# Kernel tuning notes

Measured on AMD Instinct MI355X. Metric: run time of the kernel, lower is better.

Reference implementation:

```python
import jax, jax.numpy as jnp
import numpy as np
from jax import lax

N = 2048
D_ENC = 64      # conv channels
D = 512         # node embedding dim (resnet18 feature dim)
K = 5           # max_num_neighbors
L_LAYERS = 4    # num_layers
ARENA = 32.0    # positions scaled to [0, ARENA)^2
R2 = 2.0        # radius^2 = (sqrt(2))^2


def setup_inputs() -> dict:
    key = jax.random.key(0)
    ks = jax.random.split(key, 9)
    imgs = jax.random.normal(ks[0], (N, 3, 64, 64), dtype=jnp.float32)
    pos = jax.random.uniform(ks[1], (N, 2), dtype=jnp.float32)  # scaled by ARENA inside
    conv_w = jax.random.normal(ks[2], (D_ENC, 3, 7, 7), dtype=jnp.float32) * 0.05
    conv_b = jnp.zeros((D_ENC,), dtype=jnp.float32)
    proj_w = jax.random.normal(ks[3], (D_ENC, D), dtype=jnp.float32) * (1.0 / np.sqrt(D_ENC))
    proj_b = jnp.zeros((D,), dtype=jnp.float32)
    w_self = jax.random.normal(ks[4], (L_LAYERS, D, D), dtype=jnp.float32) * (1.0 / np.sqrt(D))
    w_nbr = jax.random.normal(ks[5], (L_LAYERS, D, D), dtype=jnp.float32) * (1.0 / np.sqrt(D))
    b_gnn = jnp.zeros((L_LAYERS, D), dtype=jnp.float32)
    return {"imgs": imgs, "pos": pos, "conv_w": conv_w, "conv_b": conv_b,
            "proj_w": proj_w, "proj_b": proj_b,
            "w_self": w_self, "w_nbr": w_nbr, "b_gnn": b_gnn}


def _encode(imgs, conv_w, conv_b, proj_w, proj_b):
    # conv 7x7 stride 2 + relu + global avg pool + linear -> [N, D]
    x = lax.conv_general_dilated(imgs, conv_w, window_strides=(2, 2), padding="SAME",
                                 dimension_numbers=("NCHW", "OIHW", "NCHW"))
    x = jax.nn.relu(x + conv_b[None, :, None, None])
    x = x.mean(axis=(2, 3))                      # [N, D_ENC]
    return jax.nn.relu(x @ proj_w + proj_b)      # [N, D]


def _radius_knn(pos):
    # radius graph with radius sqrt(2), no self loops, capped at K neighbors
    p = pos * ARENA                              # [N, 2]
    d2 = jnp.sum((p[:, None, :] - p[None, :, :]) ** 2, axis=-1)  # [N, N]
    invalid = (d2 > R2) | jnp.eye(N, dtype=bool)
    d2m = jnp.where(invalid, jnp.inf, d2)
    neg_vals, idx = lax.top_k(-d2m, K)           # K nearest within radius
    valid = jnp.isfinite(neg_vals)               # [N, K]
    return idx, valid


def reference(imgs, pos, conv_w, conv_b, proj_w, proj_b, w_self, w_nbr, b_gnn):
    h = _encode(imgs, conv_w, conv_b, proj_w, proj_b)   # [N, D]
    idx, valid = _radius_knn(pos)                        # [N, K], [N, K]
    vmask = valid.astype(h.dtype)                        # [N, K]
    denom = jnp.maximum(vmask.sum(axis=1, keepdims=True), 1.0)  # [N, 1]
    for l in range(L_LAYERS):
        nbr = h[idx] * vmask[:, :, None]                 # [N, K, D] gather
        agg = nbr.sum(axis=1) / denom                    # mean over valid neighbors
        h = jax.nn.relu(h @ w_self[l] + agg @ w_nbr[l] + b_gnn[l])
    return h
```

## Files before the change

kernel.cpp:

```cpp
#include <hip/hip_runtime.h>


#define NNODES 2048

typedef __attribute__((ext_vector_type(8))) _Float16 half8;
typedef __attribute__((ext_vector_type(16))) float f32x16;

__device__ inline uint pack2h(float x, float y) {
  ushort a = __builtin_bit_cast(ushort, (_Float16)x);
  ushort b = __builtin_bit_cast(ushort, (_Float16)y);
  return (uint)a | ((uint)b << 16);
}

__global__ __launch_bounds__(256) void setup_kernel(
    const float* __restrict__ conv_w, const float* __restrict__ wsrc_s,
    const float* __restrict__ wsrc_n, const float* __restrict__ pos,
    ushort* __restrict__ wfrag, ushort* __restrict__ wT,
    int* __restrict__ nbr, float* __restrict__ den, float* __restrict__ enc) {
  __shared__ float4 smem4[1040];
  const int bid = blockIdx.x;
  const int tid = threadIdx.x;

  if (bid < 48) {
    int i = bid * 256 + tid;
    int j = i & 7;
    int l = (i >> 3) & 63;
    int q = i >> 9;
    int kb = q % 12, ct = q / 12;
    int g = 2 * kb + (l >> 5);
    int c = 32 * ct + (l & 31);
    float val = 0.f;
    if (g < 21 && j < 7) val = conv_w[c * 147 + g * 7 + j];
    wfrag[i] = __builtin_bit_cast(ushort, (_Float16)val);
    return;
  }

  if (bid < 560) {
    float(*s)[65] = (float(*)[65])smem4;
    int bid2 = bid - 48;
    int m = bid2 >> 6, kt = (bid2 >> 3) & 7, nt = bid2 & 7;
    const float* in = (m < 4) ? (wsrc_s + m * 262144) : (wsrc_n + (m - 4) * 262144);
    ushort* out = wT + m * 262144;
    int k0 = kt << 6, n0 = nt << 6;
#pragma unroll
    for (int rep = 0; rep < 4; ++rep) {
      int row = (rep << 4) + (tid >> 4);
      int c4 = (tid & 15) << 2;
      float4 v = *(const float4*)&in[(k0 + row) * 512 + n0 + c4];
      s[row][c4] = v.x; s[row][c4 + 1] = v.y; s[row][c4 + 2] = v.z; s[row][c4 + 3] = v.w;
    }
    __syncthreads();
#pragma unroll
    for (int rep = 0; rep < 4; ++rep) {
      int n = (rep << 4) + (tid >> 4);
      int k4 = (tid & 15) << 2;
      ushort4 o;
      o.x = __builtin_bit_cast(ushort, (_Float16)s[k4 + 0][n]);
      o.y = __builtin_bit_cast(ushort, (_Float16)s[k4 + 1][n]);
      o.z = __builtin_bit_cast(ushort, (_Float16)s[k4 + 2][n]);
      o.w = __builtin_bit_cast(ushort, (_Float16)s[k4 + 3][n]);
      *(ushort4*)&out[(n0 + n) * 512 + k0 + k4] = o;
    }
    return;
  }

  {
    float* s_d2 = (float*)smem4;
    int* s_idx = (int*)(s_d2 + NNODES);
    int* s_cnt = (int*)(s_idx + NNODES);
    const int i = bid - 560;
    if (tid < 16) {
      float4 z4 = {0.f, 0.f, 0.f, 0.f};
      ((float4*)(enc + i * 64))[tid] = z4;
    }
    if (tid == 0) *s_cnt = 0;
    __syncthreads();
    const float px = pos[2 * i] * 32.f, py = pos[2 * i + 1] * 32.f;
#pragma unroll
    for (int r = 0; r < 8; ++r) {
      int j = tid + (r << 8);
      float2 q = ((const float2*)pos)[j];
      float dx = q.x * 32.f - px, dy = q.y * 32.f - py;
      float d2 = dx * dx + dy * dy;
      if (d2 <= 2.0f && j != i) {
        int slot = atomicAdd(s_cnt, 1);
        s_d2[slot] = d2;
        s_idx[slot] = j;
      }
    }
    __syncthreads();
    if (tid < 64) {
      const int lane = tid;
      const int cnt = *s_cnt;
      int nf = 0;
#pragma unroll
      for (int k = 0; k < 5; ++k) {
        float best = 1e30f;
        int bslot = 0x7fffffff;
        for (int e = lane; e < cnt; e += 64) {
          float d = s_d2[e];
          if (d < best) { best = d; bslot = e; }
        }
#pragma unroll
        for (int off = 1; off < 64; off <<= 1) {
          float od = __shfl_xor(best, off);
          int os = __shfl_xor(bslot, off);
          if (od < best || (od == best && os < bslot)) { best = od; bslot = os; }
        }
        bool got = (best < 1e30f);
        if (lane == 0) nbr[i * 5 + k] = got ? s_idx[bslot] : -1;
        if (got) { s_d2[bslot] = 1e30f; ++nf; }
      }
      if (lane == 0) den[i] = 1.f / (float)(nf > 0 ? nf : 1);
    }
  }
}

__global__ __launch_bounds__(256, 3) void conv_pool_kernel(
    const float* __restrict__ imgs, const ushort* __restrict__ wfrag,
    const float* __restrict__ cb, float* __restrict__ enc) {
  __shared__ int4 s_all[2599];
  ushort* s_img = (ushort*)s_all;
  const half8* swf8 = (const half8*)((char*)s_all + 15984);
  float* s_pool = (float*)((char*)s_all + 40560);

  const int n = blockIdx.x >> 1;
  const int r0half = blockIdx.x & 1;
  const int wy = 32 * r0half - 2;
  const int tid = threadIdx.x;
  const int lane = tid & 63;
  const int w = tid >> 6;
  const int hi = lane >> 5;
  const int lo = lane & 31;

  int4 z = {0, 0, 0, 0};
  for (int i = tid; i < 999; i += 256) s_all[i] = z;
  __syncthreads();

  const int4* wf4 = (const int4*)wfrag;
  int4* swf4 = (int4*)((char*)s_all + 15984);
#pragma unroll
  for (int r = 0; r < 6; ++r) swf4[tid + r * 256] = wf4[tid + r * 256];

  const float4* src = (const float4*)(imgs + (size_t)n * 12288);
  for (int i = tid; i < 1776; i += 256) {
    int ic = i / 592;
    int rem = i - ic * 592;
    int li = rem >> 4, xq = rem & 15;
    int iy = wy + li;
    if (iy >= 0 && iy < 64) {
      float4 v = src[(ic * 64 + iy) * 16 + xq];
      int d = (ic * 37 + li) * 72 + (xq << 2) + 2;
      ((uint*)s_img)[d >> 1] = pack2h(v.x, v.y);
      ((uint*)s_img)[(d >> 1) + 1] = pack2h(v.z, v.w);
    }
  }

  int aoff[12];
#pragma unroll
  for (int kb = 0; kb < 12; ++kb) {
    int g = 2 * kb + hi;
    if (g > 20) g = 20;
    int ic = g / 7, ky = g - ic * 7;
    aoff[kb] = (ic * 37 + ky) * 144 + 4 * lo + w * 1152;
  }
  const float bias0 = cb[lo];
  const float bias1 = cb[32 + lo];
  float pool0 = 0.f, pool1 = 0.f;
  __syncthreads();

  const char* sb = (const char*)s_img;
  union F { half8 v; uint u[4]; };

#define LOADF(F0, F1, B0, B1, KB, TPADD) do {                       \
    const char* p_ = sb + aoff[KB] + (TPADD);                       \
    F0.u[0] = *(const uint*)(p_);       F0.u[1] = *(const uint*)(p_ + 4);   \
    F0.u[2] = *(const uint*)(p_ + 8);   F0.u[3] = *(const uint*)(p_ + 12);  \
    F1.u[0] = *(const uint*)(p_ + 288); F1.u[1] = *(const uint*)(p_ + 292); \
    F1.u[2] = *(const uint*)(p_ + 296); F1.u[3] = *(const uint*)(p_ + 300); \
    B0 = swf8[(KB) * 64 + lane];        B1 = swf8[(12 + (KB)) * 64 + lane]; \
  } while (0)

#pragma unroll
  for (int tp = 0; tp < 2; ++tp) {
    const int tpadd = tp * 576;
    f32x16 a0 = {}, a1 = {}, a2 = {}, a3 = {};
    F f0a, f1a, f0b, f1b;
    half8 b0a, b1a, b0b, b1b;
    LOADF(f0a, f1a, b0a, b1a, 0, tpadd);
#pragma unroll
    for (int kb = 0; kb < 12; kb += 2) {
      LOADF(f0b, f1b, b0b, b1b, kb + 1, tpadd);
      a0 = __builtin_amdgcn_mfma_f32_32x32x16_f16(f0a.v, b0a, a0, 0, 0, 0);
      a1 = __builtin_amdgcn_mfma_f32_32x32x16_f16(f0a.v, b1a, a1, 0, 0, 0);
      a2 = __builtin_amdgcn_mfma_f32_32x32x16_f16(f1a.v, b0a, a2, 0, 0, 0);
      a3 = __builtin_amdgcn_mfma_f32_32x32x16_f16(f1a.v, b1a, a3, 0, 0, 0);
      if (kb + 2 < 12) LOADF(f0a, f1a, b0a, b1a, kb + 2, tpadd);
      a0 = __builtin_amdgcn_mfma_f32_32x32x16_f16(f0b.v, b0b, a0, 0, 0, 0);
      a1 = __builtin_amdgcn_mfma_f32_32x32x16_f16(f0b.v, b1b, a1, 0, 0, 0);
      a2 = __builtin_amdgcn_mfma_f32_32x32x16_f16(f1b.v, b0b, a2, 0, 0, 0);
      a3 = __builtin_amdgcn_mfma_f32_32x32x16_f16(f1b.v, b1b, a3, 0, 0, 0);
    }
    float s0 = 0.f, s1 = 0.f;
#pragma unroll
    for (int r = 0; r < 16; ++r) {
      s0 += fmaxf(a0[r] + bias0, 0.f) + fmaxf(a2[r] + bias0, 0.f);
      s1 += fmaxf(a1[r] + bias1, 0.f) + fmaxf(a3[r] + bias1, 0.f);
    }
    pool0 += s0;
    pool1 += s1;
  }
#undef LOADF

  pool0 += __shfl_xor(pool0, 32);
  pool1 += __shfl_xor(pool1, 32);
  if (lane < 32) {
    s_pool[w * 64 + lo] = pool0;
    s_pool[w * 64 + 32 + lo] = pool1;
  }
  __syncthreads();
  if (tid < 64) {
    float s = s_pool[tid] + s_pool[64 + tid] + s_pool[128 + tid] + s_pool[192 + tid];
    atomicAdd(&enc[n * 64 + tid], s * (1.f / 1024.f));
  }
}

__global__ __launch_bounds__(256) void proj_kernel(
    const float* __restrict__ enc, const float* __restrict__ pw,
    const float* __restrict__ pb, ushort* __restrict__ h16) {
  int c = ((blockIdx.x & 1) << 8) | threadIdx.x;
  int r0 = (blockIdx.x >> 1) << 3;
  float bias = pb[c];
  float acc[8];
#pragma unroll
  for (int r = 0; r < 8; ++r) acc[r] = bias;
#pragma unroll 4
  for (int k = 0; k < 64; ++k) {
    float w = pw[k * 512 + c];
#pragma unroll
    for (int r = 0; r < 8; ++r) acc[r] = fmaf(enc[(r0 + r) * 64 + k], w, acc[r]);
  }
#pragma unroll
  for (int r = 0; r < 8; ++r)
    h16[(r0 + r) * 512 + c] = __builtin_bit_cast(ushort, (_Float16)fmaxf(acc[r], 0.f));
}

__global__ __launch_bounds__(256) void gnn_gemm_kernel(
    const ushort* __restrict__ h16, const int* __restrict__ nbr,
    const float* __restrict__ den,
    const ushort* __restrict__ Ws, const ushort* __restrict__ Wn,
    const float* __restrict__ bias, ushort* __restrict__ hout,
    float* __restrict__ fout, int final_layer) {
  __shared__ ushort s_lds[2][16384];
  __shared__ int s_nbr[320];
  __shared__ float s_den[64];
  const int tid = threadIdx.x;
  const int lane = tid & 63;
  const int hi = lane >> 5, lo = lane & 31;
  const int wu = __builtin_amdgcn_readfirstlane(tid >> 6);
  const int wr = wu >> 1, wc = wu & 1;
  const int bm = blockIdx.x >> 3, bn = blockIdx.x & 7;
  const int r0 = bm << 6, c0 = bn << 6;

  if (tid < 80) ((int4*)s_nbr)[tid] = ((const int4*)(nbr + r0 * 5))[tid];
  else if (tid < 96) ((float4*)s_den)[tid - 80] = ((const float4*)(den + r0))[tid - 80];
  __syncthreads();

  const int grow = tid >> 2, gseg = tid & 3;
  int gj[5];
  uint gm[5];
#pragma unroll
  for (int k = 0; k < 5; ++k) {
    int j = s_nbr[grow * 5 + k];
    gm[k] = (j >= 0) ? 0xFFFFFFFFu : 0u;
    gj[k] = (j >= 0) ? j : 0;
  }
  half8 den8;
  {
    _Float16 dh = (_Float16)s_den[grow];
#pragma unroll
    for (int e = 0; e < 8; ++e) den8[e] = dh;
  }

  union GU { half8 v; uint u[4]; };
  GU ga[5][2];

  auto GATHER = [&](int it) {
    const ushort* hb = h16 + (it << 6) + gseg * 16;
#pragma unroll
    for (int k = 0; k < 5; ++k) {
      const half8* p = (const half8*)(hb + gj[k] * 512);
      ga[k][0].v = p[0];
      ga[k][1].v = p[1];
    }
  };
  auto COMBINE = [&](int buf) {
#pragma unroll
    for (int part = 0; part < 2; ++part) {
      GU t0, t1, t2, t3, t4;
#pragma unroll
      for (int j2 = 0; j2 < 4; ++j2) {
        t0.u[j2] = ga[0][part].u[j2] & gm[0];
        t1.u[j2] = ga[1][part].u[j2] & gm[1];
        t2.u[j2] = ga[2][part].u[j2] & gm[2];
        t3.u[j2] = ga[3][part].u[j2] & gm[3];
        t4.u[j2] = ga[4][part].u[j2] & gm[4];
      }
      half8 s = ((t0.v + t1.v) + (t2.v + t3.v)) + t4.v;
      s = s * den8;
      *(half8*)&s_lds[buf][4096 + (2 * gseg + part) * 512 + grow * 8] = s;
    }
  };
  auto STAGE = [&](int buf, int it) {
    int k0 = it << 6;
    const ushort* ph = h16 + (r0 + lane) * 512 + k0 + 8 * wu;
    const ushort* ps = Ws + (c0 + lane) * 512 + k0 + 8 * wu;
    const ushort* pn = Wn + (c0 + lane) * 512 + k0 + 8 * wu;
    ushort* lb = &s_lds[buf][wu << 9];
#define GLDS(SRC, DST) __builtin_amdgcn_global_load_lds( \
      (const __attribute__((address_space(1))) void*)(SRC), \
      (__attribute__((address_space(3))) void*)(DST), 16, 0, 0)
    GLDS(ph, lb);            GLDS(ph + 32, lb + 2048);
    GLDS(ps, lb + 8192);     GLDS(ps + 32, lb + 10240);
    GLDS(pn, lb + 12288);    GLDS(pn + 32, lb + 14336);
#undef GLDS
  };

  f32x16 accS = {}, accN = {};
  GATHER(0);
  STAGE(0, 0);
  COMBINE(0);
  __syncthreads();
  int cur = 0;
  for (int it = 0; it < 8; ++it) {
    if (it < 7) {
      GATHER(it + 1);
      STAGE(cur ^ 1, it + 1);
    }
    const half8* pAh = (const half8*)&s_lds[cur][0];
    const half8* pAg = (const half8*)&s_lds[cur][4096];
    const half8* pBs = (const half8*)&s_lds[cur][8192];
    const half8* pBn = (const half8*)&s_lds[cur][12288];
#pragma unroll
    for (int ks = 0; ks < 4; ++ks) {
      int gi = (2 * ks + hi) * 64;
      half8 ah = pAh[gi + 32 * wr + lo];
      half8 bs = pBs[gi + 32 * wc + lo];
      accS = __builtin_amdgcn_mfma_f32_32x32x16_f16(ah, bs, accS, 0, 0, 0);
      half8 ag = pAg[gi + 32 * wr + lo];
      half8 bn2 = pBn[gi + 32 * wc + lo];
      accN = __builtin_amdgcn_mfma_f32_32x32x16_f16(ag, bn2, accN, 0, 0, 0);
    }
    if (it < 7) COMBINE(cur ^ 1);
    __syncthreads();
    cur ^= 1;
  }

  const int col = c0 + 32 * wc + lo;
  const float b = bias[col];
#pragma unroll
  for (int r = 0; r < 16; ++r) {
    int row = r0 + 32 * wr + (r & 3) + ((r >> 2) << 3) + (hi << 2);
    float v = fmaxf(accS[r] + accN[r] + b, 0.f);
    if (final_layer) fout[row * 512 + col] = v;
    else hout[row * 512 + col] = __builtin_bit_cast(ushort, (_Float16)v);
  }
}

extern "C" void kernel_launch(void* const* d_in, const int* in_sizes, int n_in,
                              void* d_out, int out_size, void* d_ws, size_t ws_size,
                              hipStream_t stream) {
  const float* imgs   = (const float*)d_in[0];
  const float* pos    = (const float*)d_in[1];
  const float* conv_w = (const float*)d_in[2];
  const float* conv_b = (const float*)d_in[3];
  const float* proj_w = (const float*)d_in[4];
  const float* proj_b = (const float*)d_in[5];
  const float* w_self = (const float*)d_in[6];
  const float* w_nbr  = (const float*)d_in[7];
  const float* b_gnn  = (const float*)d_in[8];

  char* ws = (char*)d_ws;
  ushort* wfrag = (ushort*)(ws);
  float*  enc   = (float*) (ws + 32768);
  ushort* h16a  = (ushort*)(ws + 557056);
  ushort* h16b  = (ushort*)(ws + 2654208);
  ushort* wT16  = (ushort*)(ws + 6848512);
  int*    nbr   = (int*)   (ws + 11042816);
  float*  den   = (float*) (ws + 11083776);

  setup_kernel<<<2608, 256, 0, stream>>>(conv_w, w_self, w_nbr, pos,
                                         wfrag, wT16, nbr, den, enc);
  conv_pool_kernel<<<2 * NNODES, 256, 0, stream>>>(imgs, wfrag, conv_b, enc);
  proj_kernel<<<512, 256, 0, stream>>>(enc, proj_w, proj_b, h16a);

  for (int l = 0; l < 4; ++l) {
    ushort* hin  = (l & 1) ? h16b : h16a;
    ushort* hnew = (l & 1) ? h16a : h16b;
    gnn_gemm_kernel<<<256, 256, 0, stream>>>(
        hin, nbr, den, wT16 + l * 262144, wT16 + (4 + l) * 262144,
        b_gnn + l * 512, hnew, (float*)d_out, (l == 3) ? 1 : 0);
  }
}
```

Before: 141.7 us.

## Load GNN GEMM operands directly into registers instead of staging through LDS

In the GNN GEMM kernel, the h, W_self and W_nbr tiles are now read from global memory straight into double-buffered registers, replacing the global_load_lds staging into shared memory. Only the aggregated neighbour tile still goes through LDS. This shrinks the LDS footprint and removes the LDS reads for those operands, but each wave now loads its own copy of tiles that are shared across waves, which raises register pressure and global/L2 traffic. The conv LDS fragment loads are also rewritten as 8-byte memcpys to encourage wider ds_read instructions.

```diff
diff --git a/kernel.cpp b/kernel.cpp
--- a/kernel.cpp
+++ b/kernel.cpp
@@ -172,13 +172,14 @@
   const char* sb = (const char*)s_img;
   union F { half8 v; uint u[4]; };
 
-#define LOADF(F0, F1, B0, B1, KB, TPADD) do {                       \
-    const char* p_ = sb + aoff[KB] + (TPADD);                       \
-    F0.u[0] = *(const uint*)(p_);       F0.u[1] = *(const uint*)(p_ + 4);   \
-    F0.u[2] = *(const uint*)(p_ + 8);   F0.u[3] = *(const uint*)(p_ + 12);  \
-    F1.u[0] = *(const uint*)(p_ + 288); F1.u[1] = *(const uint*)(p_ + 292); \
-    F1.u[2] = *(const uint*)(p_ + 296); F1.u[3] = *(const uint*)(p_ + 300); \
-    B0 = swf8[(KB) * 64 + lane];        B1 = swf8[(12 + (KB)) * 64 + lane]; \
+#define LOADF(F0, F1, B0, B1, KB, TPADD) do {                                 \
+    const char* p_ = (const char*)__builtin_assume_aligned(                   \
+        sb + aoff[KB] + (TPADD), 4);                                          \
+    __builtin_memcpy(&F0.u[0], p_, 8);                                        \
+    __builtin_memcpy(&F0.u[2], p_ + 8, 8);                                    \
+    __builtin_memcpy(&F1.u[0], p_ + 288, 8);                                  \
+    __builtin_memcpy(&F1.u[2], p_ + 296, 8);                                  \
+    B0 = swf8[(KB) * 64 + lane];        B1 = swf8[(12 + (KB)) * 64 + lane];   \
   } while (0)
 
 #pragma unroll
@@ -251,7 +252,7 @@
     const ushort* __restrict__ Ws, const ushort* __restrict__ Wn,
     const float* __restrict__ bias, ushort* __restrict__ hout,
     float* __restrict__ fout, int final_layer) {
-  __shared__ ushort s_lds[2][16384];
+  __shared__ ushort s_ag[2][4096];
   __shared__ int s_nbr[320];
   __shared__ float s_den[64];
   const int tid = threadIdx.x;
@@ -308,53 +309,50 @@
       }
       half8 s = ((t0.v + t1.v) + (t2.v + t3.v)) + t4.v;
       s = s * den8;
-      *(half8*)&s_lds[buf][4096 + (2 * gseg + part) * 512 + grow * 8] = s;
+      *(half8*)&s_ag[buf][(2 * gseg + part) * 512 + grow * 8] = s;
     }
   };
-  auto STAGE = [&](int buf, int it) {
-    int k0 = it << 6;
-    const ushort* ph = h16 + (r0 + lane) * 512 + k0 + 8 * wu;
-    const ushort* ps = Ws + (c0 + lane) * 512 + k0 + 8 * wu;
-    const ushort* pn = Wn + (c0 + lane) * 512 + k0 + 8 * wu;
-    ushort* lb = &s_lds[buf][wu << 9];
-#define GLDS(SRC, DST) __builtin_amdgcn_global_load_lds( \
-      (const __attribute__((address_space(1))) void*)(SRC), \
-      (__attribute__((address_space(3))) void*)(DST), 16, 0, 0)
-    GLDS(ph, lb);            GLDS(ph + 32, lb + 2048);
-    GLDS(ps, lb + 8192);     GLDS(ps + 32, lb + 10240);
-    GLDS(pn, lb + 12288);    GLDS(pn + 32, lb + 14336);
-#undef GLDS
-  };
+
+  const ushort* pA  = h16 + (r0 + 32 * wr + lo) * 512 + 8 * hi;
+  const ushort* pBs = Ws  + (c0 + 32 * wc + lo) * 512 + 8 * hi;
+  const ushort* pBn = Wn  + (c0 + 32 * wc + lo) * 512 + 8 * hi;
+
+  half8 rA[2][4], rS[2][4], rN[2][4];
+#define LOADABR(P, IT) do {                                                   \
+    int kk_ = (IT) << 6;                                                      \
+    _Pragma("unroll")                                                         \
+    for (int ks_ = 0; ks_ < 4; ++ks_) {                                       \
+      rA[P][ks_] = *(const half8*)(pA  + kk_ + 16 * ks_);                     \
+      rS[P][ks_] = *(const half8*)(pBs + kk_ + 16 * ks_);                     \
+      rN[P][ks_] = *(const half8*)(pBn + kk_ + 16 * ks_);                     \
+    }                                                                         \
+  } while (0)
 
   f32x16 accS = {}, accN = {};
   GATHER(0);
-  STAGE(0, 0);
+  LOADABR(0, 0);
   COMBINE(0);
   __syncthreads();
   int cur = 0;
+#pragma unroll
   for (int it = 0; it < 8; ++it) {
+    const int p = it & 1;
     if (it < 7) {
       GATHER(it + 1);
-      STAGE(cur ^ 1, it + 1);
-    }
-    const half8* pAh = (const half8*)&s_lds[cur][0];
-    const half8* pAg = (const half8*)&s_lds[cur][4096];
-    const half8* pBs = (const half8*)&s_lds[cur][8192];
-    const half8* pBn = (const half8*)&s_lds[cur][12288];
+      LOADABR(1 - p, it + 1);
+    }
+    const half8* agp = (const half8*)s_ag[cur];
 #pragma unroll
     for (int ks = 0; ks < 4; ++ks) {
-      int gi = (2 * ks + hi) * 64;
-      half8 ah = pAh[gi + 32 * wr + lo];
-      half8 bs = pBs[gi + 32 * wc + lo];
-      accS = __builtin_amdgcn_mfma_f32_32x32x16_f16(ah, bs, accS, 0, 0, 0);
-      half8 ag = pAg[gi + 32 * wr + lo];
-      half8 bn2 = pBn[gi + 32 * wc + lo];
-      accN = __builtin_amdgcn_mfma_f32_32x32x16_f16(ag, bn2, accN, 0, 0, 0);
+      accS = __builtin_amdgcn_mfma_f32_32x32x16_f16(rA[p][ks], rS[p][ks], accS, 0, 0, 0);
+      half8 ag = agp[(2 * ks + hi) * 64 + 32 * wr + lo];
+      accN = __builtin_amdgcn_mfma_f32_32x32x16_f16(ag, rN[p][ks], accN, 0, 0, 0);
     }
     if (it < 7) COMBINE(cur ^ 1);
     __syncthreads();
     cur ^= 1;
   }
+#undef LOADABR
 
   const int col = c0 + 32 * wc + lo;
   const float b = bias[col];
```

Measured after the change: 151.0 us. 1.07x slower.

## Split-K the GNN GEMM into two halves with a separate reduce kernel

Applied to the files above, without the earlier changes.

The GNN layer GEMM is split along K into two halves, doubling the grid from 256 to 512 blocks so more of the device's compute units are occupied. Each half writes fp32 partial sums to a workspace buffer, and a new reduce kernel adds the two partials plus bias, applies ReLU and writes fp16 or final fp32 output. This adds an extra launch per layer and extra global traffic for the partials. The conv LDS fragment loads are also rewritten as 8-byte memcpys so the compiler can emit wider LDS reads.

```diff
diff --git a/kernel.cpp b/kernel.cpp
--- a/kernel.cpp
+++ b/kernel.cpp
@@ -172,13 +172,14 @@
   const char* sb = (const char*)s_img;
   union F { half8 v; uint u[4]; };
 
-#define LOADF(F0, F1, B0, B1, KB, TPADD) do {                       \
-    const char* p_ = sb + aoff[KB] + (TPADD);                       \
-    F0.u[0] = *(const uint*)(p_);       F0.u[1] = *(const uint*)(p_ + 4);   \
-    F0.u[2] = *(const uint*)(p_ + 8);   F0.u[3] = *(const uint*)(p_ + 12);  \
-    F1.u[0] = *(const uint*)(p_ + 288); F1.u[1] = *(const uint*)(p_ + 292); \
-    F1.u[2] = *(const uint*)(p_ + 296); F1.u[3] = *(const uint*)(p_ + 300); \
-    B0 = swf8[(KB) * 64 + lane];        B1 = swf8[(12 + (KB)) * 64 + lane]; \
+#define LOADF(F0, F1, B0, B1, KB, TPADD) do {                                 \
+    const char* p_ = (const char*)__builtin_assume_aligned(                   \
+        sb + aoff[KB] + (TPADD), 4);                                          \
+    __builtin_memcpy(&F0.u[0], p_, 8);                                        \
+    __builtin_memcpy(&F0.u[2], p_ + 8, 8);                                    \
+    __builtin_memcpy(&F1.u[0], p_ + 288, 8);                                  \
+    __builtin_memcpy(&F1.u[2], p_ + 296, 8);                                  \
+    B0 = swf8[(KB) * 64 + lane];        B1 = swf8[(12 + (KB)) * 64 + lane];   \
   } while (0)
 
 #pragma unroll
@@ -249,8 +250,7 @@
     const ushort* __restrict__ h16, const int* __restrict__ nbr,
     const float* __restrict__ den,
     const ushort* __restrict__ Ws, const ushort* __restrict__ Wn,
-    const float* __restrict__ bias, ushort* __restrict__ hout,
-    float* __restrict__ fout, int final_layer) {
+    float* __restrict__ part) {
   __shared__ ushort s_lds[2][16384];
   __shared__ int s_nbr[320];
   __shared__ float s_den[64];
@@ -259,8 +259,10 @@
   const int hi = lane >> 5, lo = lane & 31;
   const int wu = __builtin_amdgcn_readfirstlane(tid >> 6);
   const int wr = wu >> 1, wc = wu & 1;
-  const int bm = blockIdx.x >> 3, bn = blockIdx.x & 7;
+  const int split = blockIdx.x >> 8;
+  const int bm = (blockIdx.x >> 3) & 31, bn = blockIdx.x & 7;
   const int r0 = bm << 6, c0 = bn << 6;
+  const int itb = split << 2;
 
   if (tid < 80) ((int4*)s_nbr)[tid] = ((const int4*)(nbr + r0 * 5))[tid];
   else if (tid < 96) ((float4*)s_den)[tid - 80] = ((const float4*)(den + r0))[tid - 80];
@@ -296,19 +298,19 @@
   };
   auto COMBINE = [&](int buf) {
 #pragma unroll
-    for (int part = 0; part < 2; ++part) {
+    for (int part2 = 0; part2 < 2; ++part2) {
       GU t0, t1, t2, t3, t4;
 #pragma unroll
       for (int j2 = 0; j2 < 4; ++j2) {
-        t0.u[j2] = ga[0][part].u[j2] & gm[0];
-        t1.u[j2] = ga[1][part].u[j2] & gm[1];
-        t2.u[j2] = ga[2][part].u[j2] & gm[2];
-        t3.u[j2] = ga[3][part].u[j2] & gm[3];
-        t4.u[j2] = ga[4][part].u[j2] & gm[4];
+        t0.u[j2] = ga[0][part2].u[j2] & gm[0];
+        t1.u[j2] = ga[1][part2].u[j2] & gm[1];
+        t2.u[j2] = ga[2][part2].u[j2] & gm[2];
+        t3.u[j2] = ga[3][part2].u[j2] & gm[3];
+        t4.u[j2] = ga[4][part2].u[j2] & gm[4];
       }
       half8 s = ((t0.v + t1.v) + (t2.v + t3.v)) + t4.v;
       s = s * den8;
-      *(half8*)&s_lds[buf][4096 + (2 * gseg + part) * 512 + grow * 8] = s;
+      *(half8*)&s_lds[buf][4096 + (2 * gseg + part2) * 512 + grow * 8] = s;
     }
   };
   auto STAGE = [&](int buf, int it) {
@@ -327,15 +329,15 @@
   };
 
   f32x16 accS = {}, accN = {};
-  GATHER(0);
-  STAGE(0, 0);
+  GATHER(itb);
+  STAGE(0, itb);
   COMBINE(0);
   __syncthreads();
   int cur = 0;
-  for (int it = 0; it < 8; ++it) {
-    if (it < 7) {
-      GATHER(it + 1);
-      STAGE(cur ^ 1, it + 1);
+  for (int it = 0; it < 4; ++it) {
+    if (it < 3) {
+      GATHER(itb + it + 1);
+      STAGE(cur ^ 1, itb + it + 1);
     }
     const half8* pAh = (const half8*)&s_lds[cur][0];
     const half8* pAg = (const half8*)&s_lds[cur][4096];
@@ -351,19 +353,41 @@
       half8 bn2 = pBn[gi + 32 * wc + lo];
       accN = __builtin_amdgcn_mfma_f32_32x32x16_f16(ag, bn2, accN, 0, 0, 0);
     }
-    if (it < 7) COMBINE(cur ^ 1);
+    if (it < 3) COMBINE(cur ^ 1);
     __syncthreads();
     cur ^= 1;
   }
 
   const int col = c0 + 32 * wc + lo;
-  const float b = bias[col];
+  float* dst = part + (size_t)split * (NNODES * 512);
 #pragma unroll
   for (int r = 0; r < 16; ++r) {
     int row = r0 + 32 * wr + (r & 3) + ((r >> 2) << 3) + (hi << 2);
-    float v = fmaxf(accS[r] + accN[r] + b, 0.f);
-    if (final_layer) fout[row * 512 + col] = v;
-    else hout[row * 512 + col] = __builtin_bit_cast(ushort, (_Float16)v);
+    dst[row * 512 + col] = accS[r] + accN[r];
+  }
+}
+
+__global__ __launch_bounds__(256) void gnn_reduce_kernel(
+    const float* __restrict__ part, const float* __restrict__ bg,
+    ushort* __restrict__ hout, float* __restrict__ fout, int final_layer) {
+  int i = blockIdx.x * 256 + threadIdx.x;
+  float4 a = ((const float4*)part)[i];
+  float4 b = ((const float4*)part)[i + 262144];
+  float4 bb = ((const float4*)bg)[i & 127];
+  float4 o;
+  o.x = fmaxf(a.x + b.x + bb.x, 0.f);
+  o.y = fmaxf(a.y + b.y + bb.y, 0.f);
+  o.z = fmaxf(a.z + b.z + bb.z, 0.f);
+  o.w = fmaxf(a.w + b.w + bb.w, 0.f);
+  if (final_layer) {
+    ((float4*)fout)[i] = o;
+  } else {
+    ushort4 h;
+    h.x = __builtin_bit_cast(ushort, (_Float16)o.x);
+    h.y = __builtin_bit_cast(ushort, (_Float16)o.y);
+    h.z = __builtin_bit_cast(ushort, (_Float16)o.z);
+    h.w = __builtin_bit_cast(ushort, (_Float16)o.w);
+    ((ushort4*)hout)[i] = h;
   }
 }
 
@@ -388,6 +412,7 @@
   ushort* wT16  = (ushort*)(ws + 6848512);
   int*    nbr   = (int*)   (ws + 11042816);
   float*  den   = (float*) (ws + 11083776);
+  float*  part  = (float*) (ws + 11534336);
 
   setup_kernel<<<2608, 256, 0, stream>>>(conv_w, w_self, w_nbr, pos,
                                          wfrag, wT16, nbr, den, enc);
@@ -397,8 +422,9 @@
   for (int l = 0; l < 4; ++l) {
     ushort* hin  = (l & 1) ? h16b : h16a;
     ushort* hnew = (l & 1) ? h16a : h16b;
-    gnn_gemm_kernel<<<256, 256, 0, stream>>>(
-        hin, nbr, den, wT16 + l * 262144, wT16 + (4 + l) * 262144,
-        b_gnn + l * 512, hnew, (float*)d_out, (l == 3) ? 1 : 0);
-  }
-}
+    gnn_gemm_kernel<<<512, 256, 0, stream>>>(
+        hin, nbr, den, wT16 + l * 262144, wT16 + (4 + l) * 262144, part);
+    gnn_reduce_kernel<<<1024, 256, 0, stream>>>(
+        part, b_gnn + l * 512, hnew, (float*)d_out, (l == 3) ? 1 : 0);
+  }
+}
```

After: 149.3 us. 5.3% more time.

## Fuse four GNN layer launches into one cooperative kernel with grid sync

Applied to the files above, without the earlier changes.

Replaces the four per-layer GEMM launches with a single cooperative kernel that loops over the layers and uses a grid-wide barrier plus threadfence between them. The goal is to remove the launch overhead and inter-kernel gaps of three extra launches. It also rewrites the conv fragment LDS loads as 8-byte memcpy with an alignment hint, so the compiler can emit wider loads. The cost is a grid sync per layer, and the grid of 256 blocks must fit co-resident for the cooperative launch.

```diff
diff --git a/kernel.cpp b/kernel.cpp
--- a/kernel.cpp
+++ b/kernel.cpp
@@ -1,4 +1,5 @@
 #include <hip/hip_runtime.h>
+#include <hip/hip_cooperative_groups.h>
 
 
 #define NNODES 2048
@@ -172,13 +173,14 @@
   const char* sb = (const char*)s_img;
   union F { half8 v; uint u[4]; };
 
-#define LOADF(F0, F1, B0, B1, KB, TPADD) do {                       \
-    const char* p_ = sb + aoff[KB] + (TPADD);                       \
-    F0.u[0] = *(const uint*)(p_);       F0.u[1] = *(const uint*)(p_ + 4);   \
-    F0.u[2] = *(const uint*)(p_ + 8);   F0.u[3] = *(const uint*)(p_ + 12);  \
-    F1.u[0] = *(const uint*)(p_ + 288); F1.u[1] = *(const uint*)(p_ + 292); \
-    F1.u[2] = *(const uint*)(p_ + 296); F1.u[3] = *(const uint*)(p_ + 300); \
-    B0 = swf8[(KB) * 64 + lane];        B1 = swf8[(12 + (KB)) * 64 + lane]; \
+#define LOADF(F0, F1, B0, B1, KB, TPADD) do {                                 \
+    const char* p_ = (const char*)__builtin_assume_aligned(                   \
+        sb + aoff[KB] + (TPADD), 4);                                          \
+    __builtin_memcpy(&F0.u[0], p_, 8);                                        \
+    __builtin_memcpy(&F0.u[2], p_ + 8, 8);                                    \
+    __builtin_memcpy(&F1.u[0], p_ + 288, 8);                                  \
+    __builtin_memcpy(&F1.u[2], p_ + 296, 8);                                  \
+    B0 = swf8[(KB) * 64 + lane];        B1 = swf8[(12 + (KB)) * 64 + lane];   \
   } while (0)
 
 #pragma unroll
@@ -245,12 +247,11 @@
     h16[(r0 + r) * 512 + c] = __builtin_bit_cast(ushort, (_Float16)fmaxf(acc[r], 0.f));
 }
 
-__global__ __launch_bounds__(256) void gnn_gemm_kernel(
-    const ushort* __restrict__ h16, const int* __restrict__ nbr,
-    const float* __restrict__ den,
-    const ushort* __restrict__ Ws, const ushort* __restrict__ Wn,
-    const float* __restrict__ bias, ushort* __restrict__ hout,
-    float* __restrict__ fout, int final_layer) {
+__global__ __launch_bounds__(256) void gnn_layers_kernel(
+    ushort* __restrict__ h16a, ushort* __restrict__ h16b,
+    const int* __restrict__ nbr, const float* __restrict__ den,
+    const ushort* __restrict__ wT16, const float* __restrict__ b_gnn,
+    float* __restrict__ fout) {
   __shared__ ushort s_lds[2][16384];
   __shared__ int s_nbr[320];
   __shared__ float s_den[64];
@@ -285,85 +286,100 @@
   union GU { half8 v; uint u[4]; };
   GU ga[5][2];
 
-  auto GATHER = [&](int it) {
-    const ushort* hb = h16 + (it << 6) + gseg * 16;
-#pragma unroll
-    for (int k = 0; k < 5; ++k) {
-      const half8* p = (const half8*)(hb + gj[k] * 512);
-      ga[k][0].v = p[0];
-      ga[k][1].v = p[1];
-    }
-  };
-  auto COMBINE = [&](int buf) {
-#pragma unroll
-    for (int part = 0; part < 2; ++part) {
-      GU t0, t1, t2, t3, t4;
-#pragma unroll
-      for (int j2 = 0; j2 < 4; ++j2) {
-        t0.u[j2] = ga[0][part].u[j2] & gm[0];
-        t1.u[j2] = ga[1][part].u[j2] & gm[1];
-        t2.u[j2] = ga[2][part].u[j2] & gm[2];
-        t3.u[j2] = ga[3][part].u[j2] & gm[3];
-        t4.u[j2] = ga[4][part].u[j2] & gm[4];
-      }
-      half8 s = ((t0.v + t1.v) + (t2.v + t3.v)) + t4.v;
-      s = s * den8;
-      *(half8*)&s_lds[buf][4096 + (2 * gseg + part) * 512 + grow * 8] = s;
-    }
-  };
-  auto STAGE = [&](int buf, int it) {
-    int k0 = it << 6;
-    const ushort* ph = h16 + (r0 + lane) * 512 + k0 + 8 * wu;
-    const ushort* ps = Ws + (c0 + lane) * 512 + k0 + 8 * wu;
-    const ushort* pn = Wn + (c0 + lane) * 512 + k0 + 8 * wu;
-    ushort* lb = &s_lds[buf][wu << 9];
+#pragma unroll 1
+  for (int l = 0; l < 4; ++l) {
+    const ushort* h16 = (l & 1) ? h16b : h16a;
+    ushort* hout = (l & 1) ? h16a : h16b;
+    const ushort* Ws = wT16 + l * 262144;
+    const ushort* Wn = wT16 + (4 + l) * 262144;
+    const float* bias = b_gnn + l * 512;
+    const int final_layer = (l == 3);
+
+    auto GATHER = [&](int it) {
+      const ushort* hb = h16 + (it << 6) + gseg * 16;
+#pragma unroll
+      for (int k = 0; k < 5; ++k) {
+        const half8* p = (const half8*)(hb + gj[k] * 512);
+        ga[k][0].v = p[0];
+        ga[k][1].v = p[1];
+      }
+    };
+    auto COMBINE = [&](int buf) {
+#pragma unroll
+      for (int part = 0; part < 2; ++part) {
+        GU t0, t1, t2, t3, t4;
+#pragma unroll
+        for (int j2 = 0; j2 < 4; ++j2) {
+          t0.u[j2] = ga[0][part].u[j2] & gm[0];
+          t1.u[j2] = ga[1][part].u[j2] & gm[1];
+          t2.u[j2] = ga[2][part].u[j2] & gm[2];
+          t3.u[j2] = ga[3][part].u[j2] & gm[3];
+          t4.u[j2] = ga[4][part].u[j2] & gm[4];
+        }
+        half8 s = ((t0.v + t1.v) + (t2.v + t3.v)) + t4.v;
+        s = s * den8;
+        *(half8*)&s_lds[buf][4096 + (2 * gseg + part) * 512 + grow * 8] = s;
+      }
+    };
+    auto STAGE = [&](int buf, int it) {
+      int k0 = it << 6;
+      const ushort* ph = h16 + (r0 + lane) * 512 + k0 + 8 * wu;
+      const ushort* ps = Ws + (c0 + lane) * 512 + k0 + 8 * wu;
+      const ushort* pn = Wn + (c0 + lane) * 512 + k0 + 8 * wu;
+      ushort* lb = &s_lds[buf][wu << 9];
 #define GLDS(SRC, DST) __builtin_amdgcn_global_load_lds( \
-      (const __attribute__((address_space(1))) void*)(SRC), \
-      (__attribute__((address_space(3))) void*)(DST), 16, 0, 0)
-    GLDS(ph, lb);            GLDS(ph + 32, lb + 2048);
-    GLDS(ps, lb + 8192);     GLDS(ps + 32, lb + 10240);
-    GLDS(pn, lb + 12288);    GLDS(pn + 32, lb + 14336);
+        (const __attribute__((address_space(1))) void*)(SRC), \
+        (__attribute__((address_space(3))) void*)(DST), 16, 0, 0)
+      GLDS(ph, lb);            GLDS(ph + 32, lb + 2048);
+      GLDS(ps, lb + 8192);     GLDS(ps + 32, lb + 10240);
+      GLDS(pn, lb + 12288);    GLDS(pn + 32, lb + 14336);
 #undef GLDS
-  };
-
-  f32x16 accS = {}, accN = {};
-  GATHER(0);
-  STAGE(0, 0);
-  COMBINE(0);
-  __syncthreads();
-  int cur = 0;
-  for (int it = 0; it < 8; ++it) {
-    if (it < 7) {
-      GATHER(it + 1);
-      STAGE(cur ^ 1, it + 1);
-    }
-    const half8* pAh = (const half8*)&s_lds[cur][0];
-    const half8* pAg = (const half8*)&s_lds[cur][4096];
-    const half8* pBs = (const half8*)&s_lds[cur][8192];
-    const half8* pBn = (const half8*)&s_lds[cur][12288];
-#pragma unroll
-    for (int ks = 0; ks < 4; ++ks) {
-      int gi = (2 * ks + hi) * 64;
-      half8 ah = pAh[gi + 32 * wr + lo];
-      half8 bs = pBs[gi + 32 * wc + lo];
-      accS = __builtin_amdgcn_mfma_f32_32x32x16_f16(ah, bs, accS, 0, 0, 0);
-      half8 ag = pAg[gi + 32 * wr + lo];
-      half8 bn2 = pBn[gi + 32 * wc + lo];
-      accN = __builtin_amdgcn_mfma_f32_32x32x16_f16(ag, bn2, accN, 0, 0, 0);
-    }
-    if (it < 7) COMBINE(cur ^ 1);
+    };
+
+    f32x16 accS = {}, accN = {};
+    GATHER(0);
+    STAGE(0, 0);
+    COMBINE(0);
     __syncthreads();
-    cur ^= 1;
-  }
-
-  const int col = c0 + 32 * wc + lo;
-  const float b = bias[col];
-#pragma unroll
-  for (int r = 0; r < 16; ++r) {
-    int row = r0 + 32 * wr + (r & 3) + ((r >> 2) << 3) + (hi << 2);
-    float v = fmaxf(accS[r] + accN[r] + b, 0.f);
-    if (final_layer) fout[row * 512 + col] = v;
-    else hout[row * 512 + col] = __builtin_bit_cast(ushort, (_Float16)v);
+    int cur = 0;
+    for (int it = 0; it < 8; ++it) {
+      if (it < 7) {
+        GATHER(it + 1);
+        STAGE(cur ^ 1, it + 1);
+      }
+      const half8* pAh = (const half8*)&s_lds[cur][0];
+      const half8* pAg = (const half8*)&s_lds[cur][4096];
+      const half8* pBs = (const half8*)&s_lds[cur][8192];
+      const half8* pBn = (const half8*)&s_lds[cur][12288];
+#pragma unroll
+      for (int ks = 0; ks < 4; ++ks) {
+        int gi = (2 * ks + hi) * 64;
+        half8 ah = pAh[gi + 32 * wr + lo];
+        half8 bs = pBs[gi + 32 * wc + lo];
+        accS = __builtin_amdgcn_mfma_f32_32x32x16_f16(ah, bs, accS, 0, 0, 0);
+        half8 ag = pAg[gi + 32 * wr + lo];
+        half8 bn2 = pBn[gi + 32 * wc + lo];
+        accN = __builtin_amdgcn_mfma_f32_32x32x16_f16(ag, bn2, accN, 0, 0, 0);
+      }
+      if (it < 7) COMBINE(cur ^ 1);
+      __syncthreads();
+      cur ^= 1;
+    }
+
+    const int col = c0 + 32 * wc + lo;
+    const float b = bias[col];
+#pragma unroll
+    for (int r = 0; r < 16; ++r) {
+      int row = r0 + 32 * wr + (r & 3) + ((r >> 2) << 3) + (hi << 2);
+      float v = fmaxf(accS[r] + accN[r] + b, 0.f);
+      if (final_layer) fout[row * 512 + col] = v;
+      else hout[row * 512 + col] = __builtin_bit_cast(ushort, (_Float16)v);
+    }
+
+    if (l < 3) {
+      __threadfence();
+      cooperative_groups::this_grid().sync();
+    }
   }
 }
 
@@ -388,17 +404,15 @@
   ushort* wT16  = (ushort*)(ws + 6848512);
   int*    nbr   = (int*)   (ws + 11042816);
   float*  den   = (float*) (ws + 11083776);
+  float*  fout  = (float*)d_out;
 
   setup_kernel<<<2608, 256, 0, stream>>>(conv_w, w_self, w_nbr, pos,
                                          wfrag, wT16, nbr, den, enc);
   conv_pool_kernel<<<2 * NNODES, 256, 0, stream>>>(imgs, wfrag, conv_b, enc);
   proj_kernel<<<512, 256, 0, stream>>>(enc, proj_w, proj_b, h16a);
 
-  for (int l = 0; l < 4; ++l) {
-    ushort* hin  = (l & 1) ? h16b : h16a;
-    ushort* hnew = (l & 1) ? h16a : h16b;
-    gnn_gemm_kernel<<<256, 256, 0, stream>>>(
-        hin, nbr, den, wT16 + l * 262144, wT16 + (4 + l) * 262144,
-        b_gnn + l * 512, hnew, (float*)d_out, (l == 3) ? 1 : 0);
-  }
-}
+  void* args[] = {(void*)&h16a, (void*)&h16b, (void*)&nbr, (void*)&den,
+                  (void*)&wT16, (void*)&b_gnn, (void*)&fout};
+  hipLaunchCooperativeKernel((void*)gnn_layers_kernel, dim3(256), dim3(256),
+                             args, 0, stream);
+}
```

Measured after the change: 319.8 us. +125.6%, slower.
